# Optimization experiments

Hardware: AMD Instinct MI355X
Metric: run time of the kernel (lower is better)

The kernel has to match this reference:

```python
import jax, jax.numpy as jnp
import numpy as np

F, C, H, W_DIM, B = 64, 1024, 32, 32, 64

def setup_inputs() -> dict:
    key = jax.random.key(0)
    k1, k2, k3 = jax.random.split(key, 3)
    x = jax.random.normal(k1, (B, F, H, W_DIM), dtype=jnp.float32)
    # nn.Linear default init: U(-1/sqrt(in), 1/sqrt(in)) for weight [out,in] and bias
    bound = 1.0 / np.sqrt(C)
    weight = jax.random.uniform(k2, (F, C, C), minval=-bound, maxval=bound, dtype=jnp.float32)
    bias = jax.random.uniform(k3, (F, C), minval=-bound, maxval=bound, dtype=jnp.float32)
    return {"x": x, "weight": weight, "bias": bias}

def reference(x, weight, bias):
    # x: [B, F, H, W]; per-feature Linear over flattened HxW (C = H*W)
    b, f, h, w = x.shape
    xf = x.reshape(b, f, h * w)                      # [B, F, C]
    # torch Linear: y = x @ W.T + b, W is [out, in] -> contract over 'in' axis
    y = jnp.einsum('bfc,foc->bfo', xf, weight) + bias  # [B, F, C]
    return y.reshape(b, f, h, w)
```

## Files before the change

### kernel.cpp

```cpp
#include <hip/hip_runtime.h>
#include <hip/hip_bf16.h>

#define F_DIM 64
#define B_DIM 64
#define C_DIM 1024
#define BN 128
#define BK 64
#define NSTEP 32
#define THREADS 512

using f32x4  = __attribute__((ext_vector_type(4))) float;
using bf16x8 = __attribute__((ext_vector_type(8))) short;
using s16x4  = __attribute__((ext_vector_type(4))) short;

static __device__ __forceinline__ short f2bf(float f) {
    unsigned u = __float_as_uint(f);
    unsigned r = (u + 0x7fffu + ((u >> 16) & 1u)) >> 16;
    return (short)r;
}

__global__ __launch_bounds__(THREADS, 2)
void channelfc_kernel(const float* __restrict__ x,
                      const float* __restrict__ w,
                      const float* __restrict__ bias,
                      float* __restrict__ out)
{
    const int n    = blockIdx.x;
    const int xcd  = n & 7;
    const int loc  = n >> 3;
    const int f    = xcd + 8 * (loc >> 2);
    const int bx   = loc & 3;

    const int tid  = threadIdx.x;
    const int lane = tid & 63;
    const int wid  = tid >> 6;
    const int wr   = wid >> 2;
    const int wc   = wid & 3;

    __shared__ short sX[B_DIM * C_DIM];
    __shared__ short sW[2][BN * BK];

    const float* xA = x + (size_t)f * C_DIM;
    const float* wB = w + (size_t)f * C_DIM * C_DIM;

    f32x4 rwA[4], rwB[4];

    auto loadW = [&](int s, f32x4 (&r)[4]) {
        const int o0 = (bx * 2 + (s >> 4)) * BN;
        const int k0 = (s & 15) * BK;
        #pragma unroll
        for (int i = 0; i < 4; ++i) {
            int id = i * THREADS + tid, row = id >> 4, k4 = id & 15;
            r[i] = *(const f32x4*)(wB + (size_t)(o0 + row) * C_DIM + k0 + k4 * 4);
        }
    };
    auto storeW = [&](int buf, const f32x4 (&r)[4]) {
        #pragma unroll
        for (int i = 0; i < 4; ++i) {
            int id = i * THREADS + tid, row = id >> 4, k4 = id & 15;
            int byte = (k4 * 8) ^ ((row & 7) << 4);
            s16x4 v; v[0]=f2bf(r[i][0]); v[1]=f2bf(r[i][1]); v[2]=f2bf(r[i][2]); v[3]=f2bf(r[i][3]);
            *(s16x4*)((char*)&sW[buf][0] + row * 128 + byte) = v;
        }
    };

    loadW(0, rwA);
    loadW(1, rwB);
    #pragma unroll 1
    for (int c8 = 0; c8 < 4; ++c8) {
        f32x4 tx[8];
        #pragma unroll
        for (int i = 0; i < 8; ++i) {
            int id = (c8 * 8 + i) * THREADS + tid;
            int row = id >> 8, k4 = id & 255;
            tx[i] = *(const f32x4*)(xA + (size_t)row * (F_DIM * C_DIM) + k4 * 4);
        }
        #pragma unroll
        for (int i = 0; i < 8; ++i) {
            int id = (c8 * 8 + i) * THREADS + tid;
            int row = id >> 8, k4 = id & 255;
            int byte = (k4 * 8) ^ ((row & 7) << 4);
            s16x4 v; v[0]=f2bf(tx[i][0]); v[1]=f2bf(tx[i][1]); v[2]=f2bf(tx[i][2]); v[3]=f2bf(tx[i][3]);
            *(s16x4*)((char*)&sX[0] + row * 2048 + byte) = v;
        }
    }
    storeW(0, rwA);
    __syncthreads();

    f32x4 acc[2][2] = {};

    auto compute = [&](int buf, int s) {
        #pragma unroll
        for (int ks = 0; ks < 2; ++ks) {
            const int kx = (s & 15) * 128 + ks * 64 + (lane >> 4) * 16;
            const int kw = ks * 64 + (lane >> 4) * 16;
            bf16x8 af[2], bfr[2];
            #pragma unroll
            for (int mt = 0; mt < 2; ++mt) {
                int row = wr * 32 + mt * 16 + (lane & 15);
                af[mt] = *(const bf16x8*)((const char*)&sX[0] + row * 2048 + (kx ^ ((row & 7) << 4)));
            }
            #pragma unroll
            for (int nt = 0; nt < 2; ++nt) {
                int row = wc * 32 + nt * 16 + (lane & 15);
                bfr[nt] = *(const bf16x8*)((const char*)&sW[buf][0] + row * 128 + (kw ^ ((row & 7) << 4)));
            }
            #pragma unroll
            for (int mt = 0; mt < 2; ++mt)
                #pragma unroll
                for (int nt = 0; nt < 2; ++nt)
                    acc[mt][nt] = __builtin_amdgcn_mfma_f32_16x16x32_bf16(af[mt], bfr[nt], acc[mt][nt], 0, 0, 0);
        }
    };

    auto epilogue = [&](int p) {
        const int ocol0 = (bx * 2 + p) * BN;
        const int ncol_base = ocol0 + wc * 32 + (lane & 15);
        const int mrow_base = wr * 32 + (lane >> 4) * 4;
        #pragma unroll
        for (int nt = 0; nt < 2; ++nt) {
            const int o  = ncol_base + nt * 16;
            const float bv = bias[f * C_DIM + o];
            #pragma unroll
            for (int mt = 0; mt < 2; ++mt)
                #pragma unroll
                for (int r = 0; r < 4; ++r) {
                    const int b = mrow_base + mt * 16 + r;
                    out[((size_t)b * F_DIM + f) * C_DIM + o] = acc[mt][nt][r] + bv;
                }
        }
    };

    #pragma unroll 1
    for (int it = 0; it < 16; ++it) {
        const int s = 2 * it;
        if (s + 2 < NSTEP) loadW(s + 2, rwA);
        storeW(1, rwB);
        compute(0, s);
        __syncthreads();
        if (s + 3 < NSTEP) loadW(s + 3, rwB);
        if (s + 2 < NSTEP) storeW(0, rwA);
        compute(1, s + 1);
        if (s + 1 == 15) {
            epilogue(0);
            #pragma unroll
            for (int mt = 0; mt < 2; ++mt)
                #pragma unroll
                for (int nt = 0; nt < 2; ++nt)
                    acc[mt][nt] = f32x4{0.f, 0.f, 0.f, 0.f};
        }
        __syncthreads();
    }
    epilogue(1);
}

extern "C" void kernel_launch(void* const* d_in, const int* in_sizes, int n_in,
                              void* d_out, int out_size, void* d_ws, size_t ws_size,
                              hipStream_t stream) {
    const float* x    = (const float*)d_in[0];
    const float* w    = (const float*)d_in[1];
    const float* bias = (const float*)d_in[2];
    float* out        = (float*)d_out;
    channelfc_kernel<<<dim3(256), dim3(THREADS), 0, stream>>>(x, w, bias, out);
}
```

Measured before the change: 62.71 us.

## Stream weights directly into MFMA B-fragments from global, dropping LDS weight staging

Each wave now loads its weight fragments straight from global memory into registers, converts them to bf16 in place, and feeds them to MFMA. The shared-memory weight double buffer and all in-loop barriers are removed. Every wave handles 16 output columns across all 64 batch rows, so the weight tiles are no longer reused through LDS. The intent is to remove LDS write/read traffic and synchronisation on the bandwidth-bound weight stream. The cost is an uncoalesced-style per-lane global access pattern and only one block per CU, which leaves little latency hiding beyond the one-step register prefetch.

```diff
diff --git a/kernel.cpp b/kernel.cpp
--- a/kernel.cpp
+++ b/kernel.cpp
@@ -4,9 +4,6 @@
 #define F_DIM 64
 #define B_DIM 64
 #define C_DIM 1024
-#define BN 128
-#define BK 64
-#define NSTEP 32
 #define THREADS 512
 
 using f32x4  = __attribute__((ext_vector_type(4))) float;
@@ -19,7 +16,7 @@
     return (short)r;
 }
 
-__global__ __launch_bounds__(THREADS, 2)
+__global__ __launch_bounds__(THREADS, 1)
 void channelfc_kernel(const float* __restrict__ x,
                       const float* __restrict__ w,
                       const float* __restrict__ bias,
@@ -29,43 +26,31 @@
     const int xcd  = n & 7;
     const int loc  = n >> 3;
     const int f    = xcd + 8 * (loc >> 2);
-    const int bx   = loc & 3;
+    const int q    = loc & 3;
 
     const int tid  = threadIdx.x;
     const int lane = tid & 63;
     const int wid  = tid >> 6;
-    const int wr   = wid >> 2;
-    const int wc   = wid & 3;
 
     __shared__ short sX[B_DIM * C_DIM];
-    __shared__ short sW[2][BN * BK];
 
     const float* xA = x + (size_t)f * C_DIM;
-    const float* wB = w + (size_t)f * C_DIM * C_DIM;
+    const float* wF = w + (size_t)f * C_DIM * C_DIM;
 
-    f32x4 rwA[4], rwB[4];
+    f32x4 wf[4][2];
 
-    auto loadW = [&](int s, f32x4 (&r)[4]) {
-        const int o0 = (bx * 2 + (s >> 4)) * BN;
-        const int k0 = (s & 15) * BK;
-        #pragma unroll
-        for (int i = 0; i < 4; ++i) {
-            int id = i * THREADS + tid, row = id >> 4, k4 = id & 15;
-            r[i] = *(const f32x4*)(wB + (size_t)(o0 + row) * C_DIM + k0 + k4 * 4);
-        }
-    };
-    auto storeW = [&](int buf, const f32x4 (&r)[4]) {
-        #pragma unroll
-        for (int i = 0; i < 4; ++i) {
-            int id = i * THREADS + tid, row = id >> 4, k4 = id & 15;
-            int byte = (k4 * 8) ^ ((row & 7) << 4);
-            s16x4 v; v[0]=f2bf(r[i][0]); v[1]=f2bf(r[i][1]); v[2]=f2bf(r[i][2]); v[3]=f2bf(r[i][3]);
-            *(s16x4*)((char*)&sW[buf][0] + row * 128 + byte) = v;
-        }
-    };
+    const int chunk_o0_base = q * 256 + wid * 32;
+    const int lrow = lane & 15;
+    const int lcol = (lane >> 4) * 8;
 
-    loadW(0, rwA);
-    loadW(1, rwB);
+    const float* wLane0 = wF + (size_t)(chunk_o0_base + lrow) * C_DIM + lcol;
+
+    #pragma unroll
+    for (int u = 0; u < 4; ++u) {
+        wf[u][0] = *(const f32x4*)(wLane0 + u * 32);
+        wf[u][1] = *(const f32x4*)(wLane0 + u * 32 + 4);
+    }
+
     #pragma unroll 1
     for (int c8 = 0; c8 < 4; ++c8) {
         f32x4 tx[8];
@@ -84,74 +69,52 @@
             *(s16x4*)((char*)&sX[0] + row * 2048 + byte) = v;
         }
     }
-    storeW(0, rwA);
     __syncthreads();
 
-    f32x4 acc[2][2] = {};
-
-    auto compute = [&](int buf, int s) {
+    #pragma unroll 1
+    for (int c = 0; c < 2; ++c) {
+        const int o0 = chunk_o0_base + c * 16;
+        const float* wLane = wF + (size_t)(o0 + lrow) * C_DIM + lcol;
+        if (c == 1) {
+            #pragma unroll
+            for (int u = 0; u < 4; ++u) {
+                wf[u][0] = *(const f32x4*)(wLane + u * 32);
+                wf[u][1] = *(const f32x4*)(wLane + u * 32 + 4);
+            }
+        }
+        f32x4 acc[4] = {};
+        #pragma unroll 1
+        for (int kb = 0; kb < 8; ++kb) {
+            #pragma unroll
+            for (int u = 0; u < 4; ++u) {
+                const int k0 = kb * 128 + u * 32;
+                bf16x8 bw;
+                bw[0]=f2bf(wf[u][0][0]); bw[1]=f2bf(wf[u][0][1]); bw[2]=f2bf(wf[u][0][2]); bw[3]=f2bf(wf[u][0][3]);
+                bw[4]=f2bf(wf[u][1][0]); bw[5]=f2bf(wf[u][1][1]); bw[6]=f2bf(wf[u][1][2]); bw[7]=f2bf(wf[u][1][3]);
+                if (kb < 7) {
+                    wf[u][0] = *(const f32x4*)(wLane + k0 + 128);
+                    wf[u][1] = *(const f32x4*)(wLane + k0 + 128 + 4);
+                }
+                const int kbyte = k0 * 2 + (lane >> 4) * 16;
+                #pragma unroll
+                for (int mt = 0; mt < 4; ++mt) {
+                    const int row = mt * 16 + lrow;
+                    bf16x8 af = *(const bf16x8*)((const char*)&sX[0] + row * 2048 + (kbyte ^ ((row & 7) << 4)));
+                    acc[mt] = __builtin_amdgcn_mfma_f32_16x16x32_bf16(af, bw, acc[mt], 0, 0, 0);
+                }
+            }
+        }
+        const int o  = o0 + lrow;
+        const float bv = bias[f * C_DIM + o];
         #pragma unroll
-        for (int ks = 0; ks < 2; ++ks) {
-            const int kx = (s & 15) * 128 + ks * 64 + (lane >> 4) * 16;
-            const int kw = ks * 64 + (lane >> 4) * 16;
-            bf16x8 af[2], bfr[2];
+        for (int mt = 0; mt < 4; ++mt) {
             #pragma unroll
-            for (int mt = 0; mt < 2; ++mt) {
-                int row = wr * 32 + mt * 16 + (lane & 15);
-                af[mt] = *(const bf16x8*)((const char*)&sX[0] + row * 2048 + (kx ^ ((row & 7) << 4)));
+            for (int r = 0; r < 4; ++r) {
+                const int b = mt * 16 + (lane >> 4) * 4 + r;
+                out[((size_t)b * F_DIM + f) * C_DIM + o] = acc[mt][r] + bv;
             }
-            #pragma unroll
-            for (int nt = 0; nt < 2; ++nt) {
-                int row = wc * 32 + nt * 16 + (lane & 15);
-                bfr[nt] = *(const bf16x8*)((const char*)&sW[buf][0] + row * 128 + (kw ^ ((row & 7) << 4)));
-            }
-            #pragma unroll
-            for (int mt = 0; mt < 2; ++mt)
-                #pragma unroll
-                for (int nt = 0; nt < 2; ++nt)
-                    acc[mt][nt] = __builtin_amdgcn_mfma_f32_16x16x32_bf16(af[mt], bfr[nt], acc[mt][nt], 0, 0, 0);
         }
-    };
-
-    auto epilogue = [&](int p) {
-        const int ocol0 = (bx * 2 + p) * BN;
-        const int ncol_base = ocol0 + wc * 32 + (lane & 15);
-        const int mrow_base = wr * 32 + (lane >> 4) * 4;
-        #pragma unroll
-        for (int nt = 0; nt < 2; ++nt) {
-            const int o  = ncol_base + nt * 16;
-            const float bv = bias[f * C_DIM + o];
-            #pragma unroll
-            for (int mt = 0; mt < 2; ++mt)
-                #pragma unroll
-                for (int r = 0; r < 4; ++r) {
-                    const int b = mrow_base + mt * 16 + r;
-                    out[((size_t)b * F_DIM + f) * C_DIM + o] = acc[mt][nt][r] + bv;
-                }
-        }
-    };
-
-    #pragma unroll 1
-    for (int it = 0; it < 16; ++it) {
-        const int s = 2 * it;
-        if (s + 2 < NSTEP) loadW(s + 2, rwA);
-        storeW(1, rwB);
-        compute(0, s);
-        __syncthreads();
-        if (s + 3 < NSTEP) loadW(s + 3, rwB);
-        if (s + 2 < NSTEP) storeW(0, rwA);
-        compute(1, s + 1);
-        if (s + 1 == 15) {
-            epilogue(0);
-            #pragma unroll
-            for (int mt = 0; mt < 2; ++mt)
-                #pragma unroll
-                for (int nt = 0; nt < 2; ++nt)
-                    acc[mt][nt] = f32x4{0.f, 0.f, 0.f, 0.f};
-        }
-        __syncthreads();
     }
-    epilogue(1);
 }
 
 extern "C" void kernel_launch(void* const* d_in, const int* in_sizes, int n_in,
```

After: 75.30 us. 20.1% more time.
